# Kernel tuning notes

Hardware: AMD Instinct MI355X
Metric: run time of the kernel (lower is better)

## Reference

```python
import jax, jax.numpy as jnp
import numpy as np

N_NODES = 50000
N_EDGES = 800000
N_FEAT = 512
N_HID = 256
N_LAYER = 4
N_CLASS = 40


def setup_inputs() -> dict:
    key = jax.random.key(0)
    ks = jax.random.split(key, 16)
    x = jax.random.normal(ks[0], (N_NODES, N_FEAT), dtype=jnp.float32)
    edge_index = jax.random.randint(ks[1], (2, N_EDGES), 0, N_NODES, dtype=jnp.int64 if jax.config.jax_enable_x64 else jnp.int32)

    def glorot(k, fan_in, fan_out):
        lim = np.sqrt(6.0 / (fan_in + fan_out)).astype(np.float32)
        return jax.random.uniform(k, (fan_in, fan_out), jnp.float32, -lim, lim)

    in_gc_W = glorot(ks[2], N_FEAT, N_HID)
    in_gc_b = jnp.zeros((N_HID,), jnp.float32)
    in_lin_W = glorot(ks[3], N_FEAT, N_HID)
    in_lin_b = jnp.zeros((N_HID,), jnp.float32)
    # n_layer-1 = 3 hidden conv / lin pairs, stacked on leading axis
    convs_W = jnp.stack([glorot(jax.random.fold_in(ks[4], i), N_HID, N_HID) for i in range(N_LAYER - 1)])
    convs_b = jnp.zeros((N_LAYER - 1, N_HID), jnp.float32)
    lins_W = jnp.stack([glorot(jax.random.fold_in(ks[5], i), N_HID, N_HID) for i in range(N_LAYER - 1)])
    lins_b = jnp.zeros((N_LAYER - 1, N_HID), jnp.float32)
    out_W = glorot(ks[6], N_HID * N_LAYER, N_CLASS)
    out_b = jnp.zeros((N_CLASS,), jnp.float32)
    return {
        "x": x, "edge_index": edge_index,
        "in_gc_W": in_gc_W, "in_gc_b": in_gc_b,
        "in_lin_W": in_lin_W, "in_lin_b": in_lin_b,
        "convs_W": convs_W, "convs_b": convs_b,
        "lins_W": lins_W, "lins_b": lins_b,
        "out_W": out_W, "out_b": out_b,
    }


def reference(x, edge_index, in_gc_W, in_gc_b, in_lin_W, in_lin_b,
              convs_W, convs_b, lins_W, lins_b, out_W, out_b):
    src, dst = edge_index[0], edge_index[1]
    n = x.shape[0]
    # GCN symmetric normalization with self-loops: deg = 1 + in-degree
    deg = jnp.zeros((n,), jnp.float32).at[dst].add(1.0) + 1.0
    dinv = jax.lax.rsqrt(deg)
    edge_norm = dinv[src] * dinv[dst]        # [E]
    self_norm = dinv * dinv                  # [N]

    def gcn(h, W, b):
        hw = h @ W                           # [N, out]
        msg = hw[src] * edge_norm[:, None]   # gather + scale
        agg = jax.ops.segment_sum(msg, dst, num_segments=n)
        agg = agg + hw * self_norm[:, None]  # self-loop term
        return agg + b

    # inductive: GCNConv + linear residual; dropout = identity (eval mode)
    h = jax.nn.relu(gcn(x, in_gc_W, in_gc_b) + x @ in_lin_W + in_lin_b)
    xs = [h]
    for i in range(convs_W.shape[0]):
        h = jax.nn.relu(gcn(h, convs_W[i], convs_b[i]) + h @ lins_W[i] + lins_b[i])
        xs.append(h)
    # JumpingKnowledge mode='cat'
    jk = jnp.concatenate(xs, axis=-1)        # [N, n_hid * n_layer]
    return jk @ out_W + out_b
```

## Files before the change

kernel.cpp:

```cpp
#include <hip/hip_runtime.h>

typedef _Float16 half8 __attribute__((ext_vector_type(8)));
typedef _Float16 half4 __attribute__((ext_vector_type(4)));
typedef float floatx4 __attribute__((ext_vector_type(4)));

__device__ __forceinline__ void gld16(const _Float16* g, _Float16* lds_base) {
    __builtin_amdgcn_global_load_lds(
        (const __attribute__((address_space(1))) unsigned int*)g,
        (__attribute__((address_space(3))) unsigned int*)lds_base,
        16, 0, 0);
}

__global__ __launch_bounds__(256) void zero_i32(int* __restrict__ p, int n) {
    int i = blockIdx.x * 256 + threadIdx.x;
    if (i < n) p[i] = 0;
}

__global__ __launch_bounds__(256) void hist_dst(const int* __restrict__ dst,
                                                int* __restrict__ count, int E) {
    int e = blockIdx.x * 256 + threadIdx.x;
    if (e < E) atomicAdd(&count[dst[e]], 1);
}

__global__ __launch_bounds__(256) void cast_f32_f16(const float* __restrict__ in,
                                                    _Float16* __restrict__ out, int n4) {
    int i = blockIdx.x * 256 + threadIdx.x;
    if (i < n4) {
        float4 v = *(const float4*)&in[(size_t)i * 4];
        half4 h = { (_Float16)v.x, (_Float16)v.y, (_Float16)v.z, (_Float16)v.w };
        *(half4*)&out[(size_t)i * 4] = h;
    }
}

__global__ __launch_bounds__(256) void transpose_cast_tiled(
    const float* __restrict__ W, _Float16* __restrict__ WT, int K, int N)
{
    __shared__ _Float16 t[32][33];
    const int k0 = blockIdx.x * 32, n0 = blockIdx.y * 32;
    const int tx = threadIdx.x & 31, ty = threadIdx.x >> 5;
    #pragma unroll
    for (int i = 0; i < 4; ++i) {
        int k = k0 + ty + i * 8, n = n0 + tx;
        float v = (k < K && n < N) ? W[(size_t)k * N + n] : 0.0f;
        t[ty + i * 8][tx] = (_Float16)v;
    }
    __syncthreads();
    #pragma unroll
    for (int i = 0; i < 4; ++i) {
        int n = n0 + ty + i * 8, k = k0 + tx;
        if (n < N && k < K) WT[(size_t)n * K + k] = t[tx][ty + i * 8];
    }
}

__global__ __launch_bounds__(256) void scan_block(const int* __restrict__ count,
                                                  int* __restrict__ incl,
                                                  int* __restrict__ blocksum,
                                                  float* __restrict__ dinv, int n) {
    __shared__ int tmp[256];
    int t = threadIdx.x;
    int i = blockIdx.x * 256 + t;
    int v = (i < n) ? count[i] : 0;
    if (i < n) dinv[i] = rsqrtf(1.0f + (float)v);
    tmp[t] = v;
    __syncthreads();
    for (int off = 1; off < 256; off <<= 1) {
        int x = (t >= off) ? tmp[t - off] : 0;
        __syncthreads();
        tmp[t] += x;
        __syncthreads();
    }
    if (i < n) incl[i] = tmp[t];
    if (t == 255) blocksum[blockIdx.x] = tmp[255];
}

__global__ __launch_bounds__(256) void scan_top(const int* __restrict__ blocksum,
                                                int* __restrict__ blockoff, int nb) {
    __shared__ int tmp[256];
    int t = threadIdx.x;
    int v = (t < nb) ? blocksum[t] : 0;
    tmp[t] = v;
    __syncthreads();
    for (int off = 1; off < 256; off <<= 1) {
        int x = (t >= off) ? tmp[t - off] : 0;
        __syncthreads();
        tmp[t] += x;
        __syncthreads();
    }
    if (t < nb) blockoff[t] = tmp[t] - v;
}

__global__ __launch_bounds__(256) void make_rowptr(const int* __restrict__ incl,
                                                   const int* __restrict__ count,
                                                   const int* __restrict__ blockoff,
                                                   int* __restrict__ rowptr,
                                                   int* __restrict__ cursor, int n) {
    int i = blockIdx.x * 256 + threadIdx.x;
    if (i < n) {
        int r = incl[i] - count[i] + blockoff[blockIdx.x];
        rowptr[i] = r;
        cursor[i] = r;
    }
}

__global__ __launch_bounds__(256) void scatter_perm(const int* __restrict__ src,
                                                    const int* __restrict__ dst,
                                                    const float* __restrict__ dinv,
                                                    int* __restrict__ cursor,
                                                    int2* __restrict__ sorted_meta, int E) {
    int e = blockIdx.x * 256 + threadIdx.x;
    if (e < E) {
        int d = dst[e], s = src[e];
        int slot = atomicAdd(&cursor[d], 1);
        sorted_meta[slot] = make_int2(s, __float_as_int(dinv[s] * dinv[d]));
    }
}

template<bool DUAL>
__global__ __launch_bounds__(256) void gemm_mfma(
    const _Float16* __restrict__ A, int lda,
    const _Float16* __restrict__ BT, int Nrows,
    const float* __restrict__ bias0, const float* __restrict__ bias1,
    _Float16* __restrict__ lin_h, _Float16* __restrict__ hw,
    float* __restrict__ Cf, int ldc,
    int M, int K)
{
    __shared__ _Float16 As[128 * 64];
    __shared__ _Float16 Bs[128 * 64];

    const int tid  = threadIdx.x;
    const int wave = tid >> 6;
    const int lane = tid & 63;
    const int q    = lane >> 4;
    const int r    = lane & 15;

    const int wm = (wave & 1) * 64;
    const int wn = (wave >> 1) * 64;

    const int bn = blockIdx.x * 128;
    const int bm = blockIdx.y * 128;

    const int srow  = wave * 32;
    const int lrow8 = lane >> 3;
    const int cp    = lane & 7;

    floatx4 acc[4][4] = {};

    for (int k0 = 0; k0 < K; k0 += 64) {
        #pragma unroll
        for (int t = 0; t < 4; ++t) {
            int lrow = srow + t * 8 + lrow8;
            int c    = cp ^ (lrow & 7);
            int gm = bm + lrow; if (gm > M - 1) gm = M - 1;
            gld16(&A[(size_t)gm * lda + k0 + c * 8], &As[(srow + t * 8) * 64]);
            int gn = bn + lrow; if (gn > Nrows - 1) gn = Nrows - 1;
            gld16(&BT[(size_t)gn * K + k0 + c * 8], &Bs[(srow + t * 8) * 64]);
        }
        __syncthreads();

        #pragma unroll
        for (int kk = 0; kk < 2; ++kk) {
            const int sc = ((kk << 2) | q) ^ (r & 7);
            half8 af[4], bf[4];
            #pragma unroll
            for (int mi = 0; mi < 4; ++mi)
                af[mi] = *(const half8*)&As[(wm + mi * 16 + r) * 64 + sc * 8];
            #pragma unroll
            for (int ni = 0; ni < 4; ++ni)
                bf[ni] = *(const half8*)&Bs[(wn + ni * 16 + r) * 64 + sc * 8];
            #pragma unroll
            for (int mi = 0; mi < 4; ++mi)
                #pragma unroll
                for (int ni = 0; ni < 4; ++ni)
                    acc[mi][ni] = __builtin_amdgcn_mfma_f32_16x16x32_f16(
                        af[mi], bf[ni], acc[mi][ni], 0, 0, 0);
        }
        __syncthreads();
    }

    if (DUAL) {
        const bool islin = (bn < 256);
        _Float16* dstp = islin ? lin_h : hw;
        #pragma unroll
        for (int ni = 0; ni < 4; ++ni) {
            int col = bn + wn + ni * 16 + r;
            int c2  = islin ? col : col - 256;
            float badd = islin ? (bias0[col] + bias1[col]) : 0.0f;
            #pragma unroll
            for (int mi = 0; mi < 4; ++mi)
                #pragma unroll
                for (int reg = 0; reg < 4; ++reg) {
                    int gm = bm + wm + mi * 16 + q * 4 + reg;
                    if (gm < M)
                        dstp[(size_t)gm * 256 + c2] = (_Float16)(acc[mi][ni][reg] + badd);
                }
        }
    } else {
        #pragma unroll
        for (int ni = 0; ni < 4; ++ni) {
            int col = bn + wn + ni * 16 + r;
            if (col >= Nrows) continue;
            float badd = bias0 ? bias0[col] : 0.0f;
            #pragma unroll
            for (int mi = 0; mi < 4; ++mi)
                #pragma unroll
                for (int reg = 0; reg < 4; ++reg) {
                    int gm = bm + wm + mi * 16 + q * 4 + reg;
                    if (gm < M)
                        Cf[(size_t)gm * ldc + col] = acc[mi][ni][reg] + badd;
                }
        }
    }
}

__global__ __launch_bounds__(256) void aggregate_csr(
    const int* __restrict__ rowptr, const int* __restrict__ count,
    const int2* __restrict__ sorted_meta,
    const float* __restrict__ dinv,
    const _Float16* __restrict__ hw,
    const _Float16* __restrict__ lin_h,
    _Float16* __restrict__ jk_col, int n)
{
    const int bx    = blockIdx.x;
    const int xslot = bx & 7;
    const int half  = xslot >> 2;
    const int chunk = ((bx >> 3) << 2) + (xslot & 3);
    const int wave  = threadIdx.x >> 6;
    const int lane  = threadIdx.x & 63;
    const int i     = chunk * 4 + wave;
    if (i >= n) return;

    const int qw = lane >> 4;
    const int fl = lane & 15;
    const int fbase = half * 128 + fl * 8;

    const int start = rowptr[i];
    const int deg   = count[i];

    float accf[8] = {};
    if (qw == 0) {
        half8 l8 = *(const half8*)&lin_h[(size_t)i * 256 + fbase];
        #pragma unroll
        for (int t = 0; t < 8; ++t) accf[t] = (float)l8[t];
    } else if (qw == 1) {
        float di = dinv[i];
        float sn = di * di;
        half8 s8 = *(const half8*)&hw[(size_t)i * 256 + fbase];
        #pragma unroll
        for (int t = 0; t < 8; ++t) accf[t] = (float)s8[t] * sn;
    }

    for (int base = 0; base < deg; base += 64) {
        int m = deg - base;
        if (m > 64) m = 64;
        int2 meta = make_int2(0, 0);
        if (lane < m) meta = sorted_meta[start + base + lane];

        for (int j = 0; j < m; j += 16) {
            half8 hv[4];
            float nm[4];
            #pragma unroll
            for (int k2 = 0; k2 < 4; ++k2) {
                int e   = j + k2 * 4 + qw;
                int idx = (e < m) ? e : (m - 1);
                int s   = __shfl(meta.x, idx, 64);
                int nmb = __shfl(meta.y, idx, 64);
                nm[k2]  = (e < m) ? __int_as_float(nmb) : 0.0f;
                hv[k2]  = *(const half8*)&hw[(size_t)s * 256 + fbase];
            }
            #pragma unroll
            for (int k2 = 0; k2 < 4; ++k2)
                #pragma unroll
                for (int t = 0; t < 8; ++t)
                    accf[t] = fmaf((float)hv[k2][t], nm[k2], accf[t]);
        }
    }

    #pragma unroll
    for (int t = 0; t < 8; ++t) {
        accf[t] += __shfl_xor(accf[t], 16, 64);
        accf[t] += __shfl_xor(accf[t], 32, 64);
    }

    if (qw == 0) {
        half8 o;
        #pragma unroll
        for (int t = 0; t < 8; ++t) o[t] = (_Float16)fmaxf(accf[t], 0.0f);
        *(half8*)&jk_col[(size_t)i * 1024 + fbase] = o;
    }
}

extern "C" void kernel_launch(void* const* d_in, const int* in_sizes, int n_in,
                              void* d_out, int out_size, void* d_ws, size_t ws_size,
                              hipStream_t stream) {
    const float* x        = (const float*)d_in[0];
    const int*   ei       = (const int*)d_in[1];
    const float* in_gc_W  = (const float*)d_in[2];
    const float* in_gc_b  = (const float*)d_in[3];
    const float* in_lin_W = (const float*)d_in[4];
    const float* in_lin_b = (const float*)d_in[5];
    const float* convs_W  = (const float*)d_in[6];
    const float* convs_b  = (const float*)d_in[7];
    const float* lins_W   = (const float*)d_in[8];
    const float* lins_b   = (const float*)d_in[9];
    const float* out_W    = (const float*)d_in[10];
    const float* out_b    = (const float*)d_in[11];

    const int N = 50000;
    const int E = in_sizes[1] / 2;
    const int F = 512, H = 256, L = 4, NC = 40;

    const int* src = ei;
    const int* dst = ei + E;

    char* ws = (char*)d_ws;
    auto carve = [&](size_t bytes) { void* p = ws; ws += (bytes + 255) & ~(size_t)255; return p; };
    float*    dinv        = (float*)carve((size_t)N * 4);
    int*      count       = (int*)  carve((size_t)N * 4);
    int*      incl        = (int*)  carve((size_t)N * 4);
    int*      rowptr      = (int*)  carve((size_t)N * 4);
    int*      cursor      = (int*)  carve((size_t)N * 4);
    int*      blocksum    = (int*)  carve(256 * 4);
    int*      blockoff    = (int*)  carve(256 * 4);
    int2*     sorted_meta = (int2*) carve((size_t)E * 8);
    _Float16* xh          = (_Float16*)carve((size_t)N * F * 2);
    _Float16* w0comb      = (_Float16*)carve((size_t)512 * F * 2);
    _Float16* wcomb       = (_Float16*)carve((size_t)3 * 512 * H * 2);
    _Float16* outWT       = (_Float16*)carve((size_t)NC * H * L * 2);
    _Float16* lin_h       = (_Float16*)carve((size_t)N * H * 2);
    _Float16* hw          = (_Float16*)carve((size_t)N * H * 2);
    _Float16* jk_h        = (_Float16*)carve((size_t)N * H * L * 2);
    float*    out         = (float*)d_out;

    const int nbN = (N + 255) / 256;
    const int nbE = (E + 255) / 256;

    zero_i32<<<nbN, 256, 0, stream>>>(count, N);
    hist_dst<<<nbE, 256, 0, stream>>>(dst, count, E);
    scan_block<<<nbN, 256, 0, stream>>>(count, incl, blocksum, dinv, N);
    scan_top<<<1, 256, 0, stream>>>(blocksum, blockoff, nbN);
    make_rowptr<<<nbN, 256, 0, stream>>>(incl, count, blockoff, rowptr, cursor, N);
    scatter_perm<<<nbE, 256, 0, stream>>>(src, dst, dinv, cursor, sorted_meta, E);

    cast_f32_f16<<<(N * F / 4 + 255) / 256, 256, 0, stream>>>(x, xh, N * F / 4);
    {
        dim3 tg((F + 31) / 32, (H + 31) / 32);
        transpose_cast_tiled<<<tg, 256, 0, stream>>>(in_lin_W, w0comb,                F, H);
        transpose_cast_tiled<<<tg, 256, 0, stream>>>(in_gc_W,  w0comb + (size_t)H * F, F, H);
        dim3 th((H + 31) / 32, (H + 31) / 32);
        for (int l = 0; l < 3; ++l) {
            _Float16* wl = wcomb + (size_t)l * 512 * H;
            transpose_cast_tiled<<<th, 256, 0, stream>>>(lins_W  + (size_t)l * H * H, wl,                 H, H);
            transpose_cast_tiled<<<th, 256, 0, stream>>>(convs_W + (size_t)l * H * H, wl + (size_t)H * H, H, H);
        }
        dim3 to((H * L + 31) / 32, (NC + 31) / 32);
        transpose_cast_tiled<<<to, 256, 0, stream>>>(out_W, outWT, H * L, NC);
    }

    const dim3 dgrid(4, (N + 127) / 128);
    const dim3 ogrid(1, (N + 127) / 128);
    const int agg_blocks = 2 * ((N + 3) / 4);

    for (int l = 0; l < L; ++l) {
        const _Float16* Ah = (l == 0) ? xh : (jk_h + (size_t)(l - 1) * H);
        int lda            = (l == 0) ? F : H * L;
        int K              = (l == 0) ? F : H;
        const _Float16* BT = (l == 0) ? w0comb : (wcomb + (size_t)(l - 1) * 512 * H);
        const float* gcB   = (l == 0) ? in_gc_b  : (convs_b + (size_t)(l - 1) * H);
        const float* liB   = (l == 0) ? in_lin_b : (lins_b  + (size_t)(l - 1) * H);

        gemm_mfma<true><<<dgrid, 256, 0, stream>>>(Ah, lda, BT, 512, liB, gcB,
                                                   lin_h, hw, nullptr, 0, N, K);
        aggregate_csr<<<agg_blocks, 256, 0, stream>>>(rowptr, count, sorted_meta,
                                                      dinv, hw, lin_h, jk_h + (size_t)l * H, N);
    }

    gemm_mfma<false><<<ogrid, 256, 0, stream>>>(jk_h, H * L, outWT, NC, out_b, nullptr,
                                                nullptr, nullptr, out, NC, N, H * L);
}
```

Before: 725.8 us.

## Replace LDS-staged MFMA GEMM with register-direct double-buffered loads and XCD-aware tile mapping

```diff
diff --git a/kernel.cpp b/kernel.cpp
--- a/kernel.cpp
+++ b/kernel.cpp
@@ -3,13 +3,6 @@
 typedef _Float16 half8 __attribute__((ext_vector_type(8)));
 typedef _Float16 half4 __attribute__((ext_vector_type(4)));
 typedef float floatx4 __attribute__((ext_vector_type(4)));
-
-__device__ __forceinline__ void gld16(const _Float16* g, _Float16* lds_base) {
-    __builtin_amdgcn_global_load_lds(
-        (const __attribute__((address_space(1))) unsigned int*)g,
-        (__attribute__((address_space(3))) unsigned int*)lds_base,
-        16, 0, 0);
-}
 
 __global__ __launch_bounds__(256) void zero_i32(int* __restrict__ p, int n) {
     int i = blockIdx.x * 256 + threadIdx.x;
@@ -116,99 +109,111 @@
 }
 
 template<bool DUAL>
-__global__ __launch_bounds__(256) void gemm_mfma(
+__global__ __launch_bounds__(256) void gemm_reg(
     const _Float16* __restrict__ A, int lda,
-    const _Float16* __restrict__ BT, int Nrows,
+    const _Float16* __restrict__ BT, int Nrows, int K,
     const float* __restrict__ bias0, const float* __restrict__ bias1,
     _Float16* __restrict__ lin_h, _Float16* __restrict__ hw,
     float* __restrict__ Cf, int ldc,
-    int M, int K)
+    int M, int m_tiles, int n_tiles)
 {
-    __shared__ _Float16 As[128 * 64];
-    __shared__ _Float16 Bs[128 * 64];
-
-    const int tid  = threadIdx.x;
-    const int wave = tid >> 6;
-    const int lane = tid & 63;
-    const int q    = lane >> 4;
-    const int r    = lane & 15;
-
-    const int wm = (wave & 1) * 64;
-    const int wn = (wave >> 1) * 64;
-
-    const int bn = blockIdx.x * 128;
-    const int bm = blockIdx.y * 128;
-
-    const int srow  = wave * 32;
-    const int lrow8 = lane >> 3;
-    const int cp    = lane & 7;
+    const int b     = blockIdx.x;
+    const int x     = b & 7;
+    const int inner = b >> 3;
+    const int n_t   = inner % n_tiles;
+    const int m_t   = (inner / n_tiles) * 8 + x;
+    if (m_t >= m_tiles) return;
+
+    const int bm = m_t * 128, bn = n_t * 128;
+    const int wave = threadIdx.x >> 6, lane = threadIdx.x & 63;
+    const int q = lane >> 4, r = lane & 15;
+    const int wm = (wave & 1) * 64, wn = (wave >> 1) * 64;
+
+    const _Float16* ap[4];
+    const _Float16* bp[4];
+    #pragma unroll
+    for (int mi = 0; mi < 4; ++mi) {
+        int gm = bm + wm + mi * 16 + r; if (gm > M - 1) gm = M - 1;
+        ap[mi] = A + (size_t)gm * lda + q * 8;
+    }
+    #pragma unroll
+    for (int ni = 0; ni < 4; ++ni) {
+        int gn = bn + wn + ni * 16 + r; if (gn > Nrows - 1) gn = Nrows - 1;
+        bp[ni] = BT + (size_t)gn * K + q * 8;
+    }
 
     floatx4 acc[4][4] = {};
-
-    for (int k0 = 0; k0 < K; k0 += 64) {
-        #pragma unroll
-        for (int t = 0; t < 4; ++t) {
-            int lrow = srow + t * 8 + lrow8;
-            int c    = cp ^ (lrow & 7);
-            int gm = bm + lrow; if (gm > M - 1) gm = M - 1;
-            gld16(&A[(size_t)gm * lda + k0 + c * 8], &As[(srow + t * 8) * 64]);
-            int gn = bn + lrow; if (gn > Nrows - 1) gn = Nrows - 1;
-            gld16(&BT[(size_t)gn * K + k0 + c * 8], &Bs[(srow + t * 8) * 64]);
-        }
-        __syncthreads();
-
-        #pragma unroll
-        for (int kk = 0; kk < 2; ++kk) {
-            const int sc = ((kk << 2) | q) ^ (r & 7);
-            half8 af[4], bf[4];
-            #pragma unroll
-            for (int mi = 0; mi < 4; ++mi)
-                af[mi] = *(const half8*)&As[(wm + mi * 16 + r) * 64 + sc * 8];
-            #pragma unroll
-            for (int ni = 0; ni < 4; ++ni)
-                bf[ni] = *(const half8*)&Bs[(wn + ni * 16 + r) * 64 + sc * 8];
-            #pragma unroll
-            for (int mi = 0; mi < 4; ++mi)
-                #pragma unroll
-                for (int ni = 0; ni < 4; ++ni)
-                    acc[mi][ni] = __builtin_amdgcn_mfma_f32_16x16x32_f16(
-                        af[mi], bf[ni], acc[mi][ni], 0, 0, 0);
-        }
-        __syncthreads();
-    }
+    half8 a0[4], b0[4], a1[4], b1[4];
+
+#define MFMA16(AF, BF)                                                      \
+    _Pragma("unroll")                                                       \
+    for (int mi = 0; mi < 4; ++mi)                                          \
+        _Pragma("unroll")                                                   \
+        for (int ni = 0; ni < 4; ++ni)                                      \
+            acc[mi][ni] = __builtin_amdgcn_mfma_f32_16x16x32_f16(           \
+                AF[mi], BF[ni], acc[mi][ni], 0, 0, 0);
+
+    #pragma unroll
+    for (int i = 0; i < 4; ++i) { a0[i] = *(const half8*)(ap[i]); b0[i] = *(const half8*)(bp[i]); }
+
+    int k0 = 0;
+    for (; k0 < K - 64; k0 += 64) {
+        #pragma unroll
+        for (int i = 0; i < 4; ++i) { a1[i] = *(const half8*)(ap[i] + 32); b1[i] = *(const half8*)(bp[i] + 32); }
+        MFMA16(a0, b0);
+        #pragma unroll
+        for (int i = 0; i < 4; ++i) { a0[i] = *(const half8*)(ap[i] + 64); b0[i] = *(const half8*)(bp[i] + 64); }
+        MFMA16(a1, b1);
+        #pragma unroll
+        for (int i = 0; i < 4; ++i) { ap[i] += 64; bp[i] += 64; }
+    }
+    #pragma unroll
+    for (int i = 0; i < 4; ++i) { a1[i] = *(const half8*)(ap[i] + 32); b1[i] = *(const half8*)(bp[i] + 32); }
+    MFMA16(a0, b0);
+    MFMA16(a1, b1);
+#undef MFMA16
 
     if (DUAL) {
         const bool islin = (bn < 256);
         _Float16* dstp = islin ? lin_h : hw;
+        float badd[4];
         #pragma unroll
         for (int ni = 0; ni < 4; ++ni) {
             int col = bn + wn + ni * 16 + r;
-            int c2  = islin ? col : col - 256;
-            float badd = islin ? (bias0[col] + bias1[col]) : 0.0f;
+            badd[ni] = islin ? (bias0[col] + bias1[col]) : 0.0f;
+        }
+        const int cbase = islin ? (bn + wn) : (bn - 256 + wn);
+        #pragma unroll
+        for (int mi = 0; mi < 4; ++mi)
             #pragma unroll
-            for (int mi = 0; mi < 4; ++mi)
+            for (int reg = 0; reg < 4; ++reg) {
+                int gm = bm + wm + mi * 16 + q * 4 + reg;
+                if (gm >= M) continue;
                 #pragma unroll
-                for (int reg = 0; reg < 4; ++reg) {
-                    int gm = bm + wm + mi * 16 + q * 4 + reg;
-                    if (gm < M)
-                        dstp[(size_t)gm * 256 + c2] = (_Float16)(acc[mi][ni][reg] + badd);
-                }
-        }
+                for (int ni = 0; ni < 4; ++ni)
+                    dstp[(size_t)gm * 256 + cbase + ni * 16 + r] =
+                        (_Float16)(acc[mi][ni][reg] + badd[ni]);
+            }
     } else {
+        float badd[4];
         #pragma unroll
         for (int ni = 0; ni < 4; ++ni) {
             int col = bn + wn + ni * 16 + r;
-            if (col >= Nrows) continue;
-            float badd = bias0 ? bias0[col] : 0.0f;
+            badd[ni] = (bias0 && col < Nrows) ? bias0[col] : 0.0f;
+        }
+        #pragma unroll
+        for (int mi = 0; mi < 4; ++mi)
             #pragma unroll
-            for (int mi = 0; mi < 4; ++mi)
+            for (int reg = 0; reg < 4; ++reg) {
+                int gm = bm + wm + mi * 16 + q * 4 + reg;
+                if (gm >= M) continue;
                 #pragma unroll
-                for (int reg = 0; reg < 4; ++reg) {
-                    int gm = bm + wm + mi * 16 + q * 4 + reg;
-                    if (gm < M)
-                        Cf[(size_t)gm * ldc + col] = acc[mi][ni][reg] + badd;
+                for (int ni = 0; ni < 4; ++ni) {
+                    int col = bn + wn + ni * 16 + r;
+                    if (col < Nrows)
+                        Cf[(size_t)gm * ldc + col] = acc[mi][ni][reg] + badd[ni];
                 }
-        }
+            }
     }
 }
 
@@ -356,9 +361,11 @@
         transpose_cast_tiled<<<to, 256, 0, stream>>>(out_W, outWT, H * L, NC);
     }
 
-    const dim3 dgrid(4, (N + 127) / 128);
-    const dim3 ogrid(1, (N + 127) / 128);
-    const int agg_blocks = 2 * ((N + 3) / 4);
+    const int m_tiles = (N + 127) / 128;
+    const int m_grps  = (m_tiles + 7) / 8;
+    const int dual_blocks = 8 * m_grps * 4;
+    const int out_blocks  = 8 * m_grps * 1;
+    const int agg_blocks  = 2 * ((N + 3) / 4);
 
     for (int l = 0; l < L; ++l) {
         const _Float16* Ah = (l == 0) ? xh : (jk_h + (size_t)(l - 1) * H);
@@ -368,12 +375,12 @@
         const float* gcB   = (l == 0) ? in_gc_b  : (convs_b + (size_t)(l - 1) * H);
         const float* liB   = (l == 0) ? in_lin_b : (lins_b  + (size_t)(l - 1) * H);
 
-        gemm_mfma<true><<<dgrid, 256, 0, stream>>>(Ah, lda, BT, 512, liB, gcB,
-                                                   lin_h, hw, nullptr, 0, N, K);
+        gemm_reg<true><<<dual_blocks, 256, 0, stream>>>(Ah, lda, BT, 512, K, liB, gcB,
+                                                        lin_h, hw, nullptr, 0, N, m_tiles, 4);
         aggregate_csr<<<agg_blocks, 256, 0, stream>>>(rowptr, count, sorted_meta,
                                                       dinv, hw, lin_h, jk_h + (size_t)l * H, N);
     }
 
-    gemm_mfma<false><<<ogrid, 256, 0, stream>>>(jk_h, H * L, outWT, NC, out_b, nullptr,
-                                                nullptr, nullptr, out, NC, N, H * L);
-}
+    gemm_reg<false><<<out_blocks, 256, 0, stream>>>(jk_h, H * L, outWT, NC, H * L, out_b, nullptr,
+                                                    nullptr, nullptr, out, NC, N, m_tiles, 1);
+}
```

After: 855.9 us. +17.9%, slower.
